# Kernel tuning notes

Hardware: AMD Instinct MI355X
Metric: run time of the kernel (lower is better)

The kernel has to match this reference:

```python
import jax, jax.numpy as jnp
import numpy as np

DIM_NODES = 128
DIM_EDGES = 64

def rms_norm(x, weight):
    eps = jnp.finfo(x.dtype).eps  # torch nn.RMSNorm default eps
    var = jnp.mean(jnp.square(x), axis=-1, keepdims=True)
    return x * jax.lax.rsqrt(var + eps) * weight

def setup_inputs() -> dict:
    key = jax.random.key(0)
    ks = jax.random.split(key, 6)
    B, N = 2, 512
    edges = jax.random.normal(ks[0], (B, N, N, DIM_EDGES), dtype=jnp.float32)
    nodes = jax.random.normal(ks[1], (B, N, DIM_NODES), dtype=jnp.float32)
    g_node = jnp.ones((DIM_NODES,), dtype=jnp.float32)
    g_edge = jnp.ones((DIM_EDGES,), dtype=jnp.float32)
    din = 2 * DIM_NODES + DIM_EDGES
    W = jax.random.normal(ks[2], (din, DIM_EDGES), dtype=jnp.float32) / np.sqrt(din)
    b = jax.random.normal(ks[3], (DIM_EDGES,), dtype=jnp.float32) * 0.01
    return {"edges": edges, "nodes": nodes, "g_node": g_node, "g_edge": g_edge, "W": W, "b": b}

def reference(edges, nodes, g_node, g_edge, W, b):
    # RMSNorms
    nodes_n = rms_norm(nodes, g_node)          # [B, N, dn]
    edges_n = rms_norm(edges, g_edge)          # [B, N, N, de]
    dn = nodes.shape[-1]
    # Decompose Linear over concat([rows, cols, edges]) into three matmuls
    # summed via broadcasting -- same math as cat+Linear, no O(N^2 * 2dn) blowup.
    Wr, Wc, We = W[:dn], W[dn:2 * dn], W[2 * dn:]
    row_proj = jnp.einsum('bid,de->bie', nodes_n, Wr)   # [B, N, de]
    col_proj = jnp.einsum('bjd,de->bje', nodes_n, Wc)   # [B, N, de]
    edge_proj = jnp.einsum('bijd,de->bije', edges_n, We)  # [B, N, N, de]
    out = edge_proj + row_proj[:, :, None, :] + col_proj[:, None, :, :] + b
    return out
```

## Files before the change

### kernel.cpp

```cpp
#include <hip/hip_runtime.h>
#include <hip/hip_bf16.h>

#define DN 128
#define DE 64
#define NN 512

typedef __bf16 bf16x8 __attribute__((ext_vector_type(8)));
typedef float  f32x4  __attribute__((ext_vector_type(4)));

__global__ void prep_kernel(const float* __restrict__ nodes,
                            const float* __restrict__ g_node,
                            const float* __restrict__ g_edge,
                            const float* __restrict__ W,
                            const float* __restrict__ bias,
                            float* __restrict__ rp, float* __restrict__ cp,
                            __bf16* __restrict__ weg) {
    const int l = threadIdx.x;
    if (blockIdx.x == 1024) {
        const int kg = l >> 4;
        for (int kh = 0; kh < 2; ++kh)
            for (int ct = 0; ct < 4; ++ct) {
                const int f = kh * 4 + ct;
                #pragma unroll
                for (int e = 0; e < 8; ++e) {
                    const int k   = kh * 32 + (e >> 2) * 16 + kg * 4 + (e & 3);
                    const int col = ct * 16 + (l & 15);
                    weg[(f * 64 + l) * 8 + e] =
                        (__bf16)(g_edge[k] * W[(2 * DN + k) * DE + col]);
                }
            }
        return;
    }
    const int row = blockIdx.x;
    __shared__ float nn[DN];

    float x0 = nodes[row * DN + l];
    float x1 = nodes[row * DN + l + 64];
    float ssq = x0 * x0 + x1 * x1;
    #pragma unroll
    for (int m = 1; m < 64; m <<= 1) ssq += __shfl_xor(ssq, m, 64);
    float scale = rsqrtf(ssq * (1.0f / DN) + 1.1920929e-7f);
    nn[l]      = x0 * scale * g_node[l];
    nn[l + 64] = x1 * scale * g_node[l + 64];
    __syncthreads();

    float accr = bias[l];
    float accc = 0.0f;
    #pragma unroll 4
    for (int d = 0; d < DN; ++d) {
        float nd = nn[d];
        accr += nd * W[d * DE + l];
        accc += nd * W[(DN + d) * DE + l];
    }
    rp[row * DE + l] = accr;
    cp[row * DE + l] = accc;
}

__global__ __launch_bounds__(256) void main_kernel(
    const float* __restrict__ edges, const float* __restrict__ rp,
    const float* __restrict__ cp, const __bf16* __restrict__ weg,
    float* __restrict__ out) {
    const int bid  = blockIdx.x;
    const int row  = bid >> 3;
    const int w    = threadIdx.x >> 6;
    const int l    = threadIdx.x & 63;
    const int r16  = l & 15;
    const int kg   = l >> 4;
    const int jt   = (bid & 7) * 64 + w * 16;
    const int j    = jt + r16;
    const int bN   = (row >> 9) << 9;

    const float* lp = edges + ((size_t)row * NN + j) * DE + kg * 4;
    f32x4 xA = *reinterpret_cast<const f32x4*>(lp);
    f32x4 xB = *reinterpret_cast<const f32x4*>(lp + 16);
    f32x4 xC = *reinterpret_cast<const f32x4*>(lp + 32);
    f32x4 xD = *reinterpret_cast<const f32x4*>(lp + 48);

    bf16x8 wf[8];
    #pragma unroll
    for (int f = 0; f < 8; ++f)
        wf[f] = *reinterpret_cast<const bf16x8*>(weg + (f * 64 + l) * 8);

    const float* cprow = cp + (size_t)(bN + j) * DE + kg * 4;
    f32x4 cpv[4];
    #pragma unroll
    for (int c = 0; c < 4; ++c)
        cpv[c] = *reinterpret_cast<const f32x4*>(cprow + c * 16);

    f32x4 rpv[4];
    #pragma unroll
    for (int c = 0; c < 4; ++c)
        rpv[c] = *reinterpret_cast<const f32x4*>(rp + row * DE + c * 16 + kg * 4);

    float ssq = 0.0f;
    #pragma unroll
    for (int e = 0; e < 4; ++e)
        ssq += xA[e] * xA[e] + xB[e] * xB[e]
             + xC[e] * xC[e] + xD[e] * xD[e];
    ssq += __shfl_xor(ssq, 16, 64);
    ssq += __shfl_xor(ssq, 32, 64);
    const float scale = rsqrtf(ssq * (1.0f / DE) + 1.1920929e-7f);

    bf16x8 a0, a1;
    #pragma unroll
    for (int e = 0; e < 4; ++e) {
        a0[e]     = (__bf16)xA[e];
        a0[e + 4] = (__bf16)xB[e];
        a1[e]     = (__bf16)xC[e];
        a1[e + 4] = (__bf16)xD[e];
    }

    float* orow = out + ((size_t)row * NN + j) * DE + kg * 4;
    #pragma unroll
    for (int c = 0; c < 4; ++c) {
        f32x4 z = {0.f, 0.f, 0.f, 0.f};
        z = __builtin_amdgcn_mfma_f32_16x16x32_bf16(wf[c],     a0, z, 0, 0, 0);
        z = __builtin_amdgcn_mfma_f32_16x16x32_bf16(wf[4 + c], a1, z, 0, 0, 0);
        f32x4 o;
        #pragma unroll
        for (int r = 0; r < 4; ++r)
            o[r] = z[r] * scale + rpv[c][r] + cpv[c][r];
        *reinterpret_cast<f32x4*>(orow + c * 16) = o;
    }
}

extern "C" void kernel_launch(void* const* d_in, const int* in_sizes, int n_in,
                              void* d_out, int out_size, void* d_ws, size_t ws_size,
                              hipStream_t stream) {
    const float* edges  = (const float*)d_in[0];
    const float* nodes  = (const float*)d_in[1];
    const float* g_node = (const float*)d_in[2];
    const float* g_edge = (const float*)d_in[3];
    const float* W      = (const float*)d_in[4];
    const float* bias   = (const float*)d_in[5];
    float* out = (float*)d_out;

    float*  rp  = (float*)d_ws;
    float*  cp  = rp + 1024 * DE;
    __bf16* weg = (__bf16*)(cp + 1024 * DE);

    prep_kernel<<<dim3(1025), dim3(64), 0, stream>>>(nodes, g_node, g_edge, W,
                                                     bias, rp, cp, weg);
    main_kernel<<<dim3(8192), dim3(256), 0, stream>>>(edges, rp, cp, weg, out);
}
```

Measured before the change: 69.26 us.

## Stage edge tiles through swizzled LDS for coalesced loads and stores

The main kernel now loads each 64x64 edge tile into shared memory with direct global-to-LDS loads, using an XOR swizzle so that per-lane reads fit the MFMA operand layout. Output is also written back through LDS so the global stores run fully coalesced. Before, each lane issued strided 16-byte accesses across rows. The change adds two block barriers and 16KB of LDS per block, which may lower occupancy and add sync latency in a kernel that is bandwidth-bound.

```diff
diff --git a/kernel.cpp b/kernel.cpp
--- a/kernel.cpp
+++ b/kernel.cpp
@@ -60,27 +60,36 @@
     const float* __restrict__ edges, const float* __restrict__ rp,
     const float* __restrict__ cp, const __bf16* __restrict__ weg,
     float* __restrict__ out) {
-    const int bid  = blockIdx.x;
-    const int row  = bid >> 3;
-    const int w    = threadIdx.x >> 6;
-    const int l    = threadIdx.x & 63;
-    const int r16  = l & 15;
-    const int kg   = l >> 4;
-    const int jt   = (bid & 7) * 64 + w * 16;
-    const int j    = jt + r16;
-    const int bN   = (row >> 9) << 9;
+    __shared__ float lds[4096];
+    const int bid = blockIdx.x;
+    const int row = bid >> 3;
+    const int t   = threadIdx.x;
+    const int w   = t >> 6;
+    const int l   = t & 63;
+    const int r16 = l & 15;
+    const int kg  = l >> 4;
+    const int jt0 = (bid & 7) * 64;
+    const int bN  = (row >> 9) << 9;
 
-    const float* lp = edges + ((size_t)row * NN + j) * DE + kg * 4;
-    f32x4 xA = *reinterpret_cast<const f32x4*>(lp);
-    f32x4 xB = *reinterpret_cast<const f32x4*>(lp + 16);
-    f32x4 xC = *reinterpret_cast<const f32x4*>(lp + 32);
-    f32x4 xD = *reinterpret_cast<const f32x4*>(lp + 48);
+    const float* tile = edges + ((size_t)row * NN + jt0) * DE;
+
+    #pragma unroll
+    for (int i = 0; i < 4; ++i) {
+        const int C = i * 256 + t;
+        const int r = C >> 4;
+        const int q = (C & 15) ^ (r & 15);
+        __builtin_amdgcn_global_load_lds(
+            (const __attribute__((address_space(1))) void*)(tile + r * DE + q * 4),
+            (__attribute__((address_space(3))) void*)(&lds[(i * 256 + w * 64) * 4]),
+            16, 0, 0);
+    }
 
     bf16x8 wf[8];
     #pragma unroll
     for (int f = 0; f < 8; ++f)
         wf[f] = *reinterpret_cast<const bf16x8*>(weg + (f * 64 + l) * 8);
 
+    const int j = jt0 + w * 16 + r16;
     const float* cprow = cp + (size_t)(bN + j) * DE + kg * 4;
     f32x4 cpv[4];
     #pragma unroll
@@ -92,11 +101,21 @@
     for (int c = 0; c < 4; ++c)
         rpv[c] = *reinterpret_cast<const f32x4*>(rp + row * DE + c * 16 + kg * 4);
 
+    __syncthreads();
+
+    const int R = w * 16 + r16;
+    f32x4 x[4];
+    #pragma unroll
+    for (int m = 0; m < 4; ++m) {
+        const int q = (m * 4 + kg) ^ r16;
+        x[m] = *reinterpret_cast<const f32x4*>(&lds[R * 64 + q * 4]);
+    }
+
     float ssq = 0.0f;
     #pragma unroll
-    for (int e = 0; e < 4; ++e)
-        ssq += xA[e] * xA[e] + xB[e] * xB[e]
-             + xC[e] * xC[e] + xD[e] * xD[e];
+    for (int m = 0; m < 4; ++m)
+        #pragma unroll
+        for (int e = 0; e < 4; ++e) ssq += x[m][e] * x[m][e];
     ssq += __shfl_xor(ssq, 16, 64);
     ssq += __shfl_xor(ssq, 32, 64);
     const float scale = rsqrtf(ssq * (1.0f / DE) + 1.1920929e-7f);
@@ -104,13 +123,12 @@
     bf16x8 a0, a1;
     #pragma unroll
     for (int e = 0; e < 4; ++e) {
-        a0[e]     = (__bf16)xA[e];
-        a0[e + 4] = (__bf16)xB[e];
-        a1[e]     = (__bf16)xC[e];
-        a1[e + 4] = (__bf16)xD[e];
+        a0[e]     = (__bf16)x[0][e];
+        a0[e + 4] = (__bf16)x[1][e];
+        a1[e]     = (__bf16)x[2][e];
+        a1[e + 4] = (__bf16)x[3][e];
     }
 
-    float* orow = out + ((size_t)row * NN + j) * DE + kg * 4;
     #pragma unroll
     for (int c = 0; c < 4; ++c) {
         f32x4 z = {0.f, 0.f, 0.f, 0.f};
@@ -120,7 +138,20 @@
         #pragma unroll
         for (int r = 0; r < 4; ++r)
             o[r] = z[r] * scale + rpv[c][r] + cpv[c][r];
-        *reinterpret_cast<f32x4*>(orow + c * 16) = o;
+        const int qo = (c * 4 + kg) ^ r16;
+        *reinterpret_cast<f32x4*>(&lds[R * 64 + qo * 4]) = o;
+    }
+
+    __syncthreads();
+
+    float* otile = out + ((size_t)row * NN + jt0) * DE;
+    #pragma unroll
+    for (int i = 0; i < 4; ++i) {
+        const int C = i * 256 + t;
+        const int r = C >> 4;
+        const int q = (C & 15) ^ (r & 15);
+        f32x4 v = *reinterpret_cast<const f32x4*>(&lds[C * 4]);
+        *reinterpret_cast<f32x4*>(otile + r * DE + q * 4) = v;
     }
 }
 
```

Measured after the change: 61.03 us. -11.9%, faster.
